# Kernel tuning notes

Measured on AMD Instinct MI355X. Metric: run time of the kernel, lower is better.

## Reference

```python
import jax, jax.numpy as jnp
import numpy as np

MODEL_DIM = 1024
HEADS = 16
HEAD_DIM = MODEL_DIM // HEADS
OUT_DIM = 1024
B, S = 2, 2048


def setup_inputs() -> dict:
    key = jax.random.key(0)
    ks = jax.random.split(key, 10)
    scale = 1.0 / np.sqrt(MODEL_DIM)
    return {
        "query": jax.random.normal(ks[0], (B, S, MODEL_DIM), dtype=jnp.float32),
        "bank": jax.random.normal(ks[1], (B, S, MODEL_DIM), dtype=jnp.float32),
        "Wq": jax.random.normal(ks[2], (MODEL_DIM, MODEL_DIM), dtype=jnp.float32) * scale,
        "bq": jnp.zeros((MODEL_DIM,), dtype=jnp.float32),
        "Wk": jax.random.normal(ks[3], (MODEL_DIM, MODEL_DIM), dtype=jnp.float32) * scale,
        "bk": jnp.zeros((MODEL_DIM,), dtype=jnp.float32),
        "Wv": jax.random.normal(ks[4], (MODEL_DIM, MODEL_DIM), dtype=jnp.float32) * scale,
        "bv": jnp.zeros((MODEL_DIM,), dtype=jnp.float32),
        "Wo": jax.random.normal(ks[5], (OUT_DIM, MODEL_DIM), dtype=jnp.float32) * scale,
        "bo": jnp.zeros((OUT_DIM,), dtype=jnp.float32),
    }


def _split_heads(x):
    # [B, S, D] -> [B, H, S, hd]
    b, s, _ = x.shape
    return x.reshape(b, s, HEADS, HEAD_DIM).transpose(0, 2, 1, 3)


def reference(query, bank, Wq, bq, Wk, bk, Wv, bv, Wo, bo):
    # Linear projections (torch Linear: x @ W.T + b)
    q = _split_heads(query @ Wq.T + bq)  # [B,H,Sq,hd]
    k = _split_heads(bank @ Wk.T + bk)   # [B,H,Sk,hd]
    v = _split_heads(bank @ Wv.T + bv)   # [B,H,Sk,hd]
    score_scale = jnp.sqrt(jnp.float32(HEAD_DIM))
    scores = jnp.einsum("bhqd,bhkd->bhqk", q / score_scale, k)  # [B,H,Sq,Sk]
    attn = jax.nn.softmax(scores, axis=-1)
    # dropout is identity in eval-mode reference
    ctx = jnp.einsum("bhqk,bhkd->bhqd", attn, v)  # [B,H,Sq,hd]
    b, h, sq, hd = ctx.shape
    ctx = ctx.transpose(0, 2, 1, 3).reshape(b, sq, MODEL_DIM)
    return ctx @ Wo.T + bo
```

## Files before the change

### kernel.cpp

```cpp
#include <hip/hip_runtime.h>


#define BDIM   2
#define SDIM   2048
#define DDIM   1024
#define HEADS  16
#define HD     64
#define MROWS  (BDIM * SDIM)

typedef float  f32x4  __attribute__((ext_vector_type(4)));
typedef __bf16 bf16x8 __attribute__((ext_vector_type(8)));
typedef __bf16 bf16x4 __attribute__((ext_vector_type(4)));
typedef unsigned u32x4 __attribute__((ext_vector_type(4)));

#define QSCALE 0.18033688011112042f

__device__ __forceinline__ void stage16(const void* g, void* l) {
    __builtin_amdgcn_global_load_lds((const __attribute__((address_space(1))) void*)g,
                                     (__attribute__((address_space(3))) void*)l,
                                     16, 0, 0);
}

__device__ __forceinline__ float vexp2(float x) {
    float r;
    asm("v_exp_f32 %0, %1" : "=v"(r) : "v"(x));
    return r;
}
__device__ __forceinline__ unsigned pk2(float lo, float hi) {
    unsigned r;
    asm("v_cvt_pk_bf16_f32 %0, %1, %2" : "=v"(r) : "v"(lo), "v"(hi));
    return r;
}

__global__ __launch_bounds__(256) void cvt_all(
    const float* __restrict__ q, const float* __restrict__ bank,
    const float* __restrict__ Wq, const float* __restrict__ Wk,
    const float* __restrict__ Wv, const float* __restrict__ Wo,
    __bf16* __restrict__ xq, __bf16* __restrict__ xkv,
    __bf16* __restrict__ wq, __bf16* __restrict__ wk,
    __bf16* __restrict__ wv, __bf16* __restrict__ wo) {
    const int i = blockIdx.x * 256 + threadIdx.x;
    const float* in;
    __bf16* out;
    int off;
    if (i < 524288)       { in = q;    out = xq;  off = i; }
    else if (i < 1048576) { in = bank; out = xkv; off = i - 524288; }
    else {
        const int j = i - 1048576;
        const int sel = j >> 17;
        off = j & 131071;
        in  = (sel == 0) ? Wq : (sel == 1) ? Wk : (sel == 2) ? Wv : Wo;
        out = (sel == 0) ? wq : (sel == 1) ? wk : (sel == 2) ? wv : wo;
    }
    const float4* p = (const float4*)in;
    float4 a = p[2 * off];
    float4 c = p[2 * off + 1];
    bf16x8 o;
    o[0] = (__bf16)a.x; o[1] = (__bf16)a.y; o[2] = (__bf16)a.z; o[3] = (__bf16)a.w;
    o[4] = (__bf16)c.x; o[5] = (__bf16)c.y; o[6] = (__bf16)c.z; o[7] = (__bf16)c.w;
    *(bf16x8*)(out + 8 * off) = o;
}

template <int MODE>
__global__ __launch_bounds__(256) void gemm_bt(
    const __bf16* __restrict__ Aq, const __bf16* __restrict__ Akv,
    const __bf16* __restrict__ W0, const __bf16* __restrict__ W1,
    const __bf16* __restrict__ W2,
    const float* __restrict__ b0, const float* __restrict__ b1,
    const float* __restrict__ b2,
    __bf16* __restrict__ Qo, __bf16* __restrict__ Ko, __bf16* __restrict__ Vo,
    float* __restrict__ Fo) {
    constexpr int NF = 2;
    constexpr int NCOL = NF * 32;
    __shared__ __align__(16) __bf16 ldsA[128 * 32];
    __shared__ __align__(16) __bf16 ldsB[NCOL * 32];

    const int t = threadIdx.x;
    const int l = t & 63;
    const int w = t >> 6;
    const int z = (MODE == 0) ? (int)blockIdx.z : 0;

    const __bf16* A  = (MODE == 0 && z != 0) ? Akv : Aq;
    const __bf16* Wm = (z == 0) ? W0 : (z == 1 ? W1 : W2);
    const float*  bias = (z == 0) ? b0 : (z == 1 ? b1 : b2);

    const int row0 = blockIdx.x * 128;
    const int col0 = blockIdx.y * NCOL;

    const int sg = (t & 3) ^ ((t >> 3) & 3);
    const __bf16* ga = A  + (size_t)(row0 + (t >> 2)) * DDIM + sg * 8;
    const __bf16* gb = Wm + (size_t)(col0 + (t >> 2)) * DDIM + sg * 8;
    __bf16* la = ldsA + (t & ~63) * 8;
    __bf16* lb = ldsB + (t & ~63) * 8;

    const int wm = w >> 1, wn = w & 1;
    const int i15 = l & 15;
    const int q4 = l >> 4;
    const int gx = q4 ^ ((i15 >> 1) & 3);

    const int aoff = (wm * 64 + i15) * 32 + gx * 8;
    const int boff = (wn * (NF * 16) + i15) * 32 + gx * 8;

    f32x4 acc[4][NF] = {};

    for (int kb = 0; kb < DDIM; kb += 32) {
        __syncthreads();
        stage16(ga + kb,             la);
        stage16(ga + kb + 64 * DDIM, la + 2048);
        stage16(gb + kb,             lb);
        __syncthreads();

        bf16x8 af[4], bf[NF];
#pragma unroll
        for (int m = 0; m < 4; ++m) af[m] = *(const bf16x8*)(ldsA + aoff + m * 16 * 32);
#pragma unroll
        for (int n = 0; n < NF; ++n) bf[n] = *(const bf16x8*)(ldsB + boff + n * 16 * 32);
#pragma unroll
        for (int m = 0; m < 4; ++m)
#pragma unroll
            for (int n = 0; n < NF; ++n)
                acc[m][n] = __builtin_amdgcn_mfma_f32_16x16x32_bf16(af[m], bf[n], acc[m][n], 0, 0, 0);
    }

#pragma unroll
    for (int m = 0; m < 4; ++m) {
        const int rbase = row0 + wm * 64 + m * 16 + (l >> 4) * 4;
#pragma unroll
        for (int n = 0; n < NF; ++n) {
            const int col = col0 + wn * (NF * 16) + n * 16 + (l & 15);
            const float bv = bias[col];
            if constexpr (MODE == 0) {
                const int hh = col >> 6, dd = col & 63;
#pragma unroll
                for (int j = 0; j < 4; ++j) {
                    const int r = rbase + j;
                    const int b = r >> 11, s = r & 2047;
                    const float v = acc[m][n][j] + bv;
                    if (z == 0) {
                        Qo[(((b * HEADS + hh) * SDIM + s) << 6) + dd] = (__bf16)(v * QSCALE);
                    } else if (z == 1) {
                        Ko[(((b * HEADS + hh) * SDIM + s) << 6) + dd] = (__bf16)v;
                    } else {
                        Vo[(((b * HEADS + hh) * HD + dd) << 11) + s] = (__bf16)v;
                    }
                }
            } else {
#pragma unroll
                for (int j = 0; j < 4; ++j) {
                    Fo[(size_t)(rbase + j) * DDIM + col] = acc[m][n][j] + bv;
                }
            }
        }
    }
}

__global__ __launch_bounds__(512) void attn_fwd(const __bf16* __restrict__ Qb,
                                                const __bf16* __restrict__ Kb,
                                                const __bf16* __restrict__ Vtb,
                                                __bf16* __restrict__ Cb) {
    __shared__ __align__(16) __bf16 ldsK[2][2][64 * 64];
    __shared__ __align__(16) __bf16 ldsV[2][2][64 * 64];

    const int t = threadIdx.x;
    const int l = t & 63;
    const int w = t >> 6;
    const int i15 = l & 15;
    const int q4 = l >> 4;

    const int bid  = blockIdx.x;
    const int xcd  = bid & 7;
    const int wloc = bid >> 3;
    const int bh   = xcd * 4 + (wloc >> 4);
    const int qb   = wloc & 15;
    const int b    = bh >> 4;
    const int h    = bh & 15;
    const size_t base = (size_t)bh * SDIM * HD;
    const int q0 = qb * 128;

    const __bf16* qp = Qb + base + (size_t)(q0 + w * 16 + i15) * HD + q4 * 8;
    const bf16x8 qf0 = *(const bf16x8*)(qp);
    const bf16x8 qf1 = *(const bf16x8*)(qp + 32);

    const int r0 = t >> 3;
    const int sl = (t & 7) ^ (r0 & 7);
    const int sig0 = ((r0 >> 5) << 5) | (((r0 >> 2) & 3) << 3)
                   | (((r0 >> 4) & 1) << 2) | (r0 & 3);
    const __bf16* gk = Kb  + base + (size_t)sig0 * HD + sl * 8;
    const __bf16* gv = Vtb + base + (size_t)r0 * SDIM + sl * 8;
    const int wb = (t & ~63) * 8;

    const int xr = i15 & 7;
    int off[4][2];
#pragma unroll
    for (int n = 0; n < 4; ++n)
#pragma unroll
        for (int hh = 0; hh < 2; ++hh)
            off[n][hh] = (n * 16 + i15) * 64 + (((hh * 4 + q4) ^ xr) << 3);

    bf16x8 ones;
#pragma unroll
    for (int j = 0; j < 8; ++j) ones[j] = (__bf16)1.0f;

    f32x4 c[4] = {};
    f32x4 lsum = {};

    stage16(gk,           &ldsK[0][0][wb]);
    stage16(gk + 64 * HD, &ldsK[0][1][wb]);
    stage16(gv,           &ldsV[0][0][wb]);
    stage16(gv + 64,      &ldsV[0][1][wb]);

#pragma unroll 2
    for (int r = 0; r < SDIM / 128; ++r) {
        const int bb = r & 1;
        __syncthreads();

        if (r + 1 < SDIM / 128) {
            const int s0 = (r + 1) * 128;
            stage16(gk + (size_t)s0 * HD,        &ldsK[bb ^ 1][0][wb]);
            stage16(gk + (size_t)(s0 + 64) * HD, &ldsK[bb ^ 1][1][wb]);
            stage16(gv + s0,                     &ldsV[bb ^ 1][0][wb]);
            stage16(gv + s0 + 64,                &ldsV[bb ^ 1][1][wb]);
        }

        const __bf16* lk0 = &ldsK[bb][0][0];
        const __bf16* lk1 = &ldsK[bb][1][0];
        const __bf16* lv0 = &ldsV[bb][0][0];
        const __bf16* lv1 = &ldsV[bb][1][0];

        f32x4 sA[4] = {}, sB[4] = {};
        __builtin_amdgcn_s_setprio(1);
#pragma unroll
        for (int n = 0; n < 4; ++n) {
            bf16x8 k0 = *(const bf16x8*)(lk0 + off[n][0]);
            bf16x8 k1 = *(const bf16x8*)(lk0 + off[n][1]);
            sA[n] = __builtin_amdgcn_mfma_f32_16x16x32_bf16(k0, qf0, sA[n], 0, 0, 0);
            sA[n] = __builtin_amdgcn_mfma_f32_16x16x32_bf16(k1, qf1, sA[n], 0, 0, 0);
        }
#pragma unroll
        for (int n = 0; n < 4; ++n) {
            bf16x8 k0 = *(const bf16x8*)(lk1 + off[n][0]);
            bf16x8 k1 = *(const bf16x8*)(lk1 + off[n][1]);
            sB[n] = __builtin_amdgcn_mfma_f32_16x16x32_bf16(k0, qf0, sB[n], 0, 0, 0);
            sB[n] = __builtin_amdgcn_mfma_f32_16x16x32_bf16(k1, qf1, sB[n], 0, 0, 0);
        }
        __builtin_amdgcn_s_setprio(0);

#pragma unroll
        for (int n = 0; n < 4; ++n)
#pragma unroll
            for (int j = 0; j < 4; ++j) {
                sA[n][j] = vexp2(sA[n][j]);
                sB[n][j] = vexp2(sB[n][j]);
            }

        u32x4 pw0, pw1, pw2, pw3;
        pw0[0] = pk2(sA[0][0], sA[0][1]); pw0[1] = pk2(sA[0][2], sA[0][3]);
        pw0[2] = pk2(sA[1][0], sA[1][1]); pw0[3] = pk2(sA[1][2], sA[1][3]);
        pw1[0] = pk2(sA[2][0], sA[2][1]); pw1[1] = pk2(sA[2][2], sA[2][3]);
        pw1[2] = pk2(sA[3][0], sA[3][1]); pw1[3] = pk2(sA[3][2], sA[3][3]);
        pw2[0] = pk2(sB[0][0], sB[0][1]); pw2[1] = pk2(sB[0][2], sB[0][3]);
        pw2[2] = pk2(sB[1][0], sB[1][1]); pw2[3] = pk2(sB[1][2], sB[1][3]);
        pw3[0] = pk2(sB[2][0], sB[2][1]); pw3[1] = pk2(sB[2][2], sB[2][3]);
        pw3[2] = pk2(sB[3][0], sB[3][1]); pw3[3] = pk2(sB[3][2], sB[3][3]);
        const bf16x8 paA0 = __builtin_bit_cast(bf16x8, pw0);
        const bf16x8 paB0 = __builtin_bit_cast(bf16x8, pw1);
        const bf16x8 paA1 = __builtin_bit_cast(bf16x8, pw2);
        const bf16x8 paB1 = __builtin_bit_cast(bf16x8, pw3);

        __builtin_amdgcn_s_setprio(1);
        lsum = __builtin_amdgcn_mfma_f32_16x16x32_bf16(ones, paA0, lsum, 0, 0, 0);
        lsum = __builtin_amdgcn_mfma_f32_16x16x32_bf16(ones, paB0, lsum, 0, 0, 0);
        lsum = __builtin_amdgcn_mfma_f32_16x16x32_bf16(ones, paA1, lsum, 0, 0, 0);
        lsum = __builtin_amdgcn_mfma_f32_16x16x32_bf16(ones, paB1, lsum, 0, 0, 0);
#pragma unroll
        for (int n2 = 0; n2 < 4; ++n2) {
            bf16x8 v0 = *(const bf16x8*)(lv0 + off[n2][0]);
            bf16x8 v1 = *(const bf16x8*)(lv0 + off[n2][1]);
            c[n2] = __builtin_amdgcn_mfma_f32_16x16x32_bf16(v0, paA0, c[n2], 0, 0, 0);
            c[n2] = __builtin_amdgcn_mfma_f32_16x16x32_bf16(v1, paB0, c[n2], 0, 0, 0);
            bf16x8 u0 = *(const bf16x8*)(lv1 + off[n2][0]);
            bf16x8 u1 = *(const bf16x8*)(lv1 + off[n2][1]);
            c[n2] = __builtin_amdgcn_mfma_f32_16x16x32_bf16(u0, paA1, c[n2], 0, 0, 0);
            c[n2] = __builtin_amdgcn_mfma_f32_16x16x32_bf16(u1, paB1, c[n2], 0, 0, 0);
        }
        __builtin_amdgcn_s_setprio(0);
    }

    const float inv = 1.0f / lsum[0];
    const int q = q0 + w * 16 + i15;
#pragma unroll
    for (int n2 = 0; n2 < 4; ++n2) {
        bf16x4 o;
#pragma unroll
        for (int j = 0; j < 4; ++j) o[j] = (__bf16)(c[n2][j] * inv);
        *(bf16x4*)(Cb + (size_t)(b * SDIM + q) * DDIM + h * HD + n2 * 16 + q4 * 4) = o;
    }
}

extern "C" void kernel_launch(void* const* d_in, const int* in_sizes, int n_in,
                              void* d_out, int out_size, void* d_ws, size_t ws_size,
                              hipStream_t stream) {
    const float* query = (const float*)d_in[0];
    const float* bank  = (const float*)d_in[1];
    const float* Wq = (const float*)d_in[2];
    const float* bq = (const float*)d_in[3];
    const float* Wk = (const float*)d_in[4];
    const float* bk = (const float*)d_in[5];
    const float* Wv = (const float*)d_in[6];
    const float* bv = (const float*)d_in[7];
    const float* Wo = (const float*)d_in[8];
    const float* bo = (const float*)d_in[9];
    float* out = (float*)d_out;

    char* ws = (char*)d_ws;
    __bf16* xq  = (__bf16*)(ws);
    __bf16* xkv = (__bf16*)(ws + (8u  << 20));
    __bf16* wq  = (__bf16*)(ws + (16u << 20));
    __bf16* wk  = (__bf16*)(ws + (18u << 20));
    __bf16* wv  = (__bf16*)(ws + (20u << 20));
    __bf16* wo  = (__bf16*)(ws + (22u << 20));
    __bf16* qbuf = (__bf16*)(ws + (24u << 20));
    __bf16* kbuf = (__bf16*)(ws + (32u << 20));
    __bf16* vtbuf = (__bf16*)(ws + (40u << 20));
    __bf16* ctx = xq;

    cvt_all<<<6144, 256, 0, stream>>>(query, bank, Wq, Wk, Wv, Wo,
                                      xq, xkv, wq, wk, wv, wo);

    gemm_bt<0><<<dim3(32, 16, 3), 256, 0, stream>>>(
        xq, xkv, wq, wk, wv, bq, bk, bv, qbuf, kbuf, vtbuf, nullptr);

    attn_fwd<<<512, 512, 0, stream>>>(qbuf, kbuf, vtbuf, ctx);

    gemm_bt<2><<<dim3(32, 16, 1), 256, 0, stream>>>(
        ctx, nullptr, wo, nullptr, nullptr, bo, nullptr, nullptr,
        nullptr, nullptr, nullptr, out);
}
```

Before: 128.5 us.

## Retile QKV projection GEMM into 256x256 double-buffered blocks

```diff
diff --git a/kernel.cpp b/kernel.cpp
--- a/kernel.cpp
+++ b/kernel.cpp
@@ -61,35 +61,136 @@
     *(bf16x8*)(out + 8 * off) = o;
 }
 
-template <int MODE>
-__global__ __launch_bounds__(256) void gemm_bt(
+__global__ __launch_bounds__(512, 1) void gemm_qkv(
     const __bf16* __restrict__ Aq, const __bf16* __restrict__ Akv,
     const __bf16* __restrict__ W0, const __bf16* __restrict__ W1,
     const __bf16* __restrict__ W2,
     const float* __restrict__ b0, const float* __restrict__ b1,
     const float* __restrict__ b2,
-    __bf16* __restrict__ Qo, __bf16* __restrict__ Ko, __bf16* __restrict__ Vo,
-    float* __restrict__ Fo) {
-    constexpr int NF = 2;
-    constexpr int NCOL = NF * 32;
-    __shared__ __align__(16) __bf16 ldsA[128 * 32];
-    __shared__ __align__(16) __bf16 ldsB[NCOL * 32];
+    __bf16* __restrict__ Qo, __bf16* __restrict__ Ko, __bf16* __restrict__ Vo) {
+    __shared__ __align__(16) __bf16 ldsA[2][256 * 64];
+    __shared__ __align__(16) __bf16 ldsB[2][256 * 64];
 
     const int t = threadIdx.x;
     const int l = t & 63;
     const int w = t >> 6;
-    const int z = (MODE == 0) ? (int)blockIdx.z : 0;
-
-    const __bf16* A  = (MODE == 0 && z != 0) ? Akv : Aq;
+
+    const int bid = blockIdx.x;
+    const int bx  = bid & 15;
+    const int by  = (bid >> 4) & 3;
+    const int z   = bid >> 6;
+
+    const __bf16* A  = (z == 0) ? Aq : Akv;
     const __bf16* Wm = (z == 0) ? W0 : (z == 1 ? W1 : W2);
     const float*  bias = (z == 0) ? b0 : (z == 1 ? b1 : b2);
 
+    const int row0 = bx * 256;
+    const int col0 = by * 256;
+
+    const int sg = (t & 7) ^ ((t >> 3) & 7);
+    const __bf16* ga = A  + (size_t)(row0 + (t >> 3)) * DDIM + sg * 8;
+    const __bf16* gb = Wm + (size_t)(col0 + (t >> 3)) * DDIM + sg * 8;
+    const int wbase = (t & ~63) * 8;
+
+    const int wm = w >> 2, wn = w & 3;
+    const int i15 = l & 15;
+    const int q4 = l >> 4;
+    const int xr = i15 & 7;
+
+    int aoff[8][2], boff[4][2];
+#pragma unroll
+    for (int mb = 0; mb < 8; ++mb)
+#pragma unroll
+        for (int ks = 0; ks < 2; ++ks)
+            aoff[mb][ks] = (wm * 128 + mb * 16 + i15) * 64 + (((ks * 4 + q4) ^ xr) << 3);
+#pragma unroll
+    for (int nb = 0; nb < 4; ++nb)
+#pragma unroll
+        for (int ks = 0; ks < 2; ++ks)
+            boff[nb][ks] = (wn * 64 + nb * 16 + i15) * 64 + (((ks * 4 + q4) ^ xr) << 3);
+
+    f32x4 acc[8][4] = {};
+
+#define QKV_STAGE(db, kb)                                                      \
+    do {                                                                       \
+        _Pragma("unroll") for (int c = 0; c < 4; ++c)                          \
+            stage16(ga + (kb) + (size_t)(64 * c) * DDIM,                       \
+                    &ldsA[db][c * 4096 + wbase]);                              \
+        _Pragma("unroll") for (int c = 0; c < 4; ++c)                          \
+            stage16(gb + (kb) + (size_t)(64 * c) * DDIM,                       \
+                    &ldsB[db][c * 4096 + wbase]);                              \
+    } while (0)
+
+    QKV_STAGE(0, 0);
+
+#pragma unroll 2
+    for (int kt = 0; kt < 16; ++kt) {
+        const int db = kt & 1;
+        asm volatile("s_waitcnt vmcnt(0)" ::: "memory");
+        __builtin_amdgcn_s_barrier();
+        asm volatile("" ::: "memory");
+        if (kt + 1 < 16) {
+            QKV_STAGE(db ^ 1, (kt + 1) * 64);
+        }
+        const __bf16* lA = &ldsA[db][0];
+        const __bf16* lB = &ldsB[db][0];
+#pragma unroll
+        for (int ks = 0; ks < 2; ++ks) {
+            bf16x8 bf[4];
+#pragma unroll
+            for (int nb = 0; nb < 4; ++nb) bf[nb] = *(const bf16x8*)(lB + boff[nb][ks]);
+#pragma unroll
+            for (int mb = 0; mb < 8; ++mb) {
+                bf16x8 af = *(const bf16x8*)(lA + aoff[mb][ks]);
+#pragma unroll
+                for (int nb = 0; nb < 4; ++nb)
+                    acc[mb][nb] = __builtin_amdgcn_mfma_f32_16x16x32_bf16(af, bf[nb], acc[mb][nb], 0, 0, 0);
+            }
+        }
+    }
+#undef QKV_STAGE
+
+#pragma unroll
+    for (int mb = 0; mb < 8; ++mb) {
+        const int rbase = row0 + wm * 128 + mb * 16 + q4 * 4;
+#pragma unroll
+        for (int nb = 0; nb < 4; ++nb) {
+            const int col = col0 + wn * 64 + nb * 16 + i15;
+            const float bv = bias[col];
+            const int hh = col >> 6, dd = col & 63;
+#pragma unroll
+            for (int j = 0; j < 4; ++j) {
+                const int r = rbase + j;
+                const int b = r >> 11, s = r & 2047;
+                const float v = acc[mb][nb][j] + bv;
+                if (z == 0) {
+                    Qo[(((b * HEADS + hh) * SDIM + s) << 6) + dd] = (__bf16)(v * QSCALE);
+                } else if (z == 1) {
+                    Ko[(((b * HEADS + hh) * SDIM + s) << 6) + dd] = (__bf16)v;
+                } else {
+                    Vo[(((b * HEADS + hh) * HD + dd) << 11) + s] = (__bf16)v;
+                }
+            }
+        }
+    }
+}
+
+__global__ __launch_bounds__(256) void gemm_out(
+    const __bf16* __restrict__ A, const __bf16* __restrict__ W,
+    const float* __restrict__ bias, float* __restrict__ Fo) {
+    __shared__ __align__(16) __bf16 ldsA[128 * 32];
+    __shared__ __align__(16) __bf16 ldsB[64 * 32];
+
+    const int t = threadIdx.x;
+    const int l = t & 63;
+    const int w = t >> 6;
+
     const int row0 = blockIdx.x * 128;
-    const int col0 = blockIdx.y * NCOL;
+    const int col0 = blockIdx.y * 64;
 
     const int sg = (t & 3) ^ ((t >> 3) & 3);
-    const __bf16* ga = A  + (size_t)(row0 + (t >> 2)) * DDIM + sg * 8;
-    const __bf16* gb = Wm + (size_t)(col0 + (t >> 2)) * DDIM + sg * 8;
+    const __bf16* ga = A + (size_t)(row0 + (t >> 2)) * DDIM + sg * 8;
+    const __bf16* gb = W + (size_t)(col0 + (t >> 2)) * DDIM + sg * 8;
     __bf16* la = ldsA + (t & ~63) * 8;
     __bf16* lb = ldsB + (t & ~63) * 8;
 
@@ -99,9 +200,9 @@
     const int gx = q4 ^ ((i15 >> 1) & 3);
 
     const int aoff = (wm * 64 + i15) * 32 + gx * 8;
-    const int boff = (wn * (NF * 16) + i15) * 32 + gx * 8;
-
-    f32x4 acc[4][NF] = {};
+    const int boff = (wn * 32 + i15) * 32 + gx * 8;
+
+    f32x4 acc[4][2] = {};
 
     for (int kb = 0; kb < DDIM; kb += 32) {
         __syncthreads();
@@ -110,15 +211,15 @@
         stage16(gb + kb,             lb);
         __syncthreads();
 
-        bf16x8 af[4], bf[NF];
+        bf16x8 af[4], bf[2];
 #pragma unroll
         for (int m = 0; m < 4; ++m) af[m] = *(const bf16x8*)(ldsA + aoff + m * 16 * 32);
 #pragma unroll
-        for (int n = 0; n < NF; ++n) bf[n] = *(const bf16x8*)(ldsB + boff + n * 16 * 32);
+        for (int n = 0; n < 2; ++n) bf[n] = *(const bf16x8*)(ldsB + boff + n * 16 * 32);
 #pragma unroll
         for (int m = 0; m < 4; ++m)
 #pragma unroll
-            for (int n = 0; n < NF; ++n)
+            for (int n = 0; n < 2; ++n)
                 acc[m][n] = __builtin_amdgcn_mfma_f32_16x16x32_bf16(af[m], bf[n], acc[m][n], 0, 0, 0);
     }
 
@@ -126,29 +227,12 @@
     for (int m = 0; m < 4; ++m) {
         const int rbase = row0 + wm * 64 + m * 16 + (l >> 4) * 4;
 #pragma unroll
-        for (int n = 0; n < NF; ++n) {
-            const int col = col0 + wn * (NF * 16) + n * 16 + (l & 15);
+        for (int n = 0; n < 2; ++n) {
+            const int col = col0 + wn * 32 + n * 16 + (l & 15);
             const float bv = bias[col];
-            if constexpr (MODE == 0) {
-                const int hh = col >> 6, dd = col & 63;
-#pragma unroll
-                for (int j = 0; j < 4; ++j) {
-                    const int r = rbase + j;
-                    const int b = r >> 11, s = r & 2047;
-                    const float v = acc[m][n][j] + bv;
-                    if (z == 0) {
-                        Qo[(((b * HEADS + hh) * SDIM + s) << 6) + dd] = (__bf16)(v * QSCALE);
-                    } else if (z == 1) {
-                        Ko[(((b * HEADS + hh) * SDIM + s) << 6) + dd] = (__bf16)v;
-                    } else {
-                        Vo[(((b * HEADS + hh) * HD + dd) << 11) + s] = (__bf16)v;
-                    }
-                }
-            } else {
-#pragma unroll
-                for (int j = 0; j < 4; ++j) {
-                    Fo[(size_t)(rbase + j) * DDIM + col] = acc[m][n][j] + bv;
-                }
+#pragma unroll
+            for (int j = 0; j < 4; ++j) {
+                Fo[(size_t)(rbase + j) * DDIM + col] = acc[m][n][j] + bv;
             }
         }
     }
@@ -327,12 +411,10 @@
     cvt_all<<<6144, 256, 0, stream>>>(query, bank, Wq, Wk, Wv, Wo,
                                       xq, xkv, wq, wk, wv, wo);
 
-    gemm_bt<0><<<dim3(32, 16, 3), 256, 0, stream>>>(
-        xq, xkv, wq, wk, wv, bq, bk, bv, qbuf, kbuf, vtbuf, nullptr);
+    gemm_qkv<<<192, 512, 0, stream>>>(
+        xq, xkv, wq, wk, wv, bq, bk, bv, qbuf, kbuf, vtbuf);
 
     attn_fwd<<<512, 512, 0, stream>>>(qbuf, kbuf, vtbuf, ctx);
 
-    gemm_bt<2><<<dim3(32, 16, 1), 256, 0, stream>>>(
-        ctx, nullptr, wo, nullptr, nullptr, bo, nullptr, nullptr,
-        nullptr, nullptr, nullptr, out);
-}
+    gemm_out<<<dim3(32, 16), 256, 0, stream>>>(ctx, wo, bo, out);
+}
```

After: 129.6 us. Within noise of the previous version (+0.9%).
